# Kernel tuning notes

Measured on AMD Instinct MI355X. Metric: run time of the kernel, lower is better.

The kernel has to match this reference:

```python
import jax, jax.numpy as jnp
import numpy as np

TOL = 0.5          # Time_tolerance
DECAY = 1.0        # decay_rate
RES = 0.03         # integral_resolution
T_MAX = 120.0
G = 4000           # int(T_MAX / RES)


def setup_inputs() -> dict:
    key = jax.random.key(0)
    ks = jax.random.split(key, 8)
    B, N, H = 128, 64, 128
    times0 = jnp.sort(jax.random.uniform(ks[0], (B, N), dtype=jnp.float32) * T_MAX, axis=-1)
    times1 = jnp.sort(jax.random.uniform(ks[1], (B, N), dtype=jnp.float32) * T_MAX, axis=-1)
    states0 = jax.random.randint(ks[2], (B, N), 0, 2, dtype=jnp.int32)
    states1 = jax.random.randint(ks[3], (B, N), 0, 2, dtype=jnp.int32)
    head_times = jnp.sort(jax.random.uniform(ks[4], (B, H), dtype=jnp.float32) * T_MAX, axis=-1)
    head_states = jax.random.randint(ks[5], (B, H), 0, 2, dtype=jnp.int32)
    base = jnp.full((1,), -0.2, dtype=jnp.float32)  # torch.ones(1) * -0.2
    weights = jax.random.normal(ks[6], (2,), dtype=jnp.float32) * 0.1
    return dict(times0=times0, states0=states0, times1=times1, states1=states1,
                head_times=head_times, head_states=head_states, base=base, weights=weights)


def _intensity(t, times0, states0, times1, states1, head_times, head_states, base, wn):
    # t: [B,T] evaluation times; times*: [B,N]; head_*: [B,H]
    te = t[..., None]                                   # [B,T,1]
    t0 = times0[:, None, :]                             # [B,1,N]
    t1 = times1[:, None, :]
    s0 = states0[:, None, :]
    s1 = states1[:, None, :]
    # exp(-decay*(t - tau)); clamp dt>=0 so masked-out (future) events don't overflow
    dec0 = jnp.exp(-DECAY * jnp.maximum(te - t0, 0.0))  # [B,T,N]
    dec1 = jnp.exp(-DECAY * jnp.maximum(te - t1, 0.0))
    # Formula 0: body [0,1], signs [1,1], relations (0 BEFORE 1), (1 BEFORE head)
    A = jnp.where((t0 <= te) & (s0 == 1), dec0, 0.0)                 # history mask + kernel on pred0
    Bm = jnp.where((t1 < te - TOL) & (s1 == 1), dec1, 0.0)           # (t1 BEFORE head) + history mask
    M = (times0[:, :, None] - times1[:, None, :] < -TOL).astype(t.dtype)  # [B,N,N] (t0 BEFORE t1)
    feat0 = jnp.einsum('bti,bij,btj->bt', A, M, Bm)  # sum over itertools.product pairs
    # Formula 1: body [0], sign [0], relation (0 BEFORE head)
    feat1 = jnp.sum(jnp.where((t0 < te - TOL) & (s0 == 0), dec0, 0.0), axis=-1)
    # formula effect: cur_state via idx = sum(t > head_times) - 1 (numpy negative-index wrap)
    cnt = jnp.sum(te > head_times[:, None, :], axis=-1)              # [B,T]
    Hn = head_times.shape[-1]
    cur_state = jnp.take_along_axis(head_states, (cnt - 1) % Hn, axis=-1)
    eff0 = jnp.where(cur_state == 0, 1.0, -1.0).astype(t.dtype)      # head sign 1 -> +1 iff counter_state==1
    eff1 = -eff0                                                      # head sign 0
    return jnp.exp(base[0] + wn[0] * feat0 * eff0 + wn[1] * feat1 * eff1)


def reference(times0, states0, times1, states1, head_times, head_states, base, weights):
    wn = jax.nn.softmax(weights)  # exp(w)/sum exp(w)
    B = times0.shape[0]
    grid = jnp.broadcast_to((jnp.arange(G, dtype=times0.dtype) * RES)[None, :], (B, G))
    lam_grid = _intensity(grid, times0, states0, times1, states1, head_times, head_states, base, wn)
    lam_ev = _intensity(head_times[:, 1:], times0, states0, times1, states1, head_times, head_states, base, wn)
    log_sum = jnp.sum(jnp.log(lam_ev))
    integral = jnp.sum(lam_grid) * RES
    return (log_sum - integral).reshape(1)
```

## Files before the change

kernel.cpp:

```cpp
#include <hip/hip_runtime.h>
#include <math.h>

constexpr int Bb = 128;
constexpr int Nn = 64;
constexpr int Hh = 128;
constexpr int Gg = 4000;
constexpr float  TOLf = 0.5f;
constexpr double RESd = 0.03;

constexpr int GBLK  = 16;
constexpr int NGRID = Bb * GBLK;
constexpr int NBLK  = NGRID + Bb;
constexpr int TSTRIDE = 72;

__device__ __forceinline__ int lb64(const float* __restrict__ a, float key) {
    int lo = (a[31] < key) ? 32 : 0;
    lo += (a[lo + 15] < key) ? 16 : 0;
    lo += (a[lo + 7]  < key) ? 8  : 0;
    lo += (a[lo + 3]  < key) ? 4  : 0;
    lo += (a[lo + 1]  < key) ? 2  : 0;
    lo += (a[lo]      < key) ? 1  : 0;
    lo += (a[lo]      < key) ? 1  : 0;
    return lo;
}
__device__ __forceinline__ int ub64(const float* __restrict__ a, float key) {
    int lo = (a[31] <= key) ? 32 : 0;
    lo += (a[lo + 15] <= key) ? 16 : 0;
    lo += (a[lo + 7]  <= key) ? 8  : 0;
    lo += (a[lo + 3]  <= key) ? 4  : 0;
    lo += (a[lo + 1]  <= key) ? 2  : 0;
    lo += (a[lo]      <= key) ? 1  : 0;
    lo += (a[lo]      <= key) ? 1  : 0;
    return lo;
}
__device__ __forceinline__ int lb128(const float* __restrict__ a, float key) {
    int lo = (a[63] < key) ? 64 : 0;
    lo += (a[lo + 31] < key) ? 32 : 0;
    lo += (a[lo + 15] < key) ? 16 : 0;
    lo += (a[lo + 7]  < key) ? 8  : 0;
    lo += (a[lo + 3]  < key) ? 4  : 0;
    lo += (a[lo + 1]  < key) ? 2  : 0;
    lo += (a[lo]      < key) ? 1  : 0;
    lo += (a[lo]      < key) ? 1  : 0;
    return lo;
}

__global__ __launch_bounds__(64) void precompute_kernel(
    const float* __restrict__ times0, const int* __restrict__ states0,
    const float* __restrict__ times1, const int* __restrict__ states1,
    double* __restrict__ Ps_all, double* __restrict__ Qs_all,
    double* __restrict__ SW_all, double* __restrict__ SWP_all,
    int* __restrict__ kT_all)
{
    const int b = blockIdx.x;
    const int i = threadIdx.x;

    __shared__ float  t1s[Nn];
    __shared__ int    j0s[Nn];
    __shared__ double Ps_sh[Nn + 1];

    const float t0 = times0[b * Nn + i];
    const float t1 = times1[b * Nn + i];
    const int   s0 = states0[b * Nn + i];
    const int   s1 = states1[b * Nn + i];
    t1s[i] = t1;
    __syncthreads();

    int j0 = 0;
    #pragma unroll
    for (int j = 0; j < Nn; ++j)
        j0 += (t0 - t1s[j] >= -TOLf) ? 1 : 0;
    j0s[i] = j0;

    const double e0 = exp((double)t0);
    double vp = (s1 == 1) ? exp((double)t1) : 0.0;
    double vq = (s0 == 0) ? e0 : 0.0;
    const double W = (s0 == 1) ? e0 : 0.0;
    double vw = W;

    #pragma unroll
    for (int off = 1; off < 64; off <<= 1) {
        double op = __shfl_up(vp, off, 64);
        double oq = __shfl_up(vq, off, 64);
        double ow = __shfl_up(vw, off, 64);
        if (i >= off) { vp += op; vq += oq; vw += ow; }
    }
    Ps_sh[i + 1] = vp;
    if (i == 0) Ps_sh[0] = 0.0;
    __syncthreads();

    double vwp = W * Ps_sh[j0];
    #pragma unroll
    for (int off = 1; off < 64; off <<= 1) {
        double o = __shfl_up(vwp, off, 64);
        if (i >= off) vwp += o;
    }

    int kc = 0;
    #pragma unroll
    for (int j = 0; j < Nn; ++j)
        kc += (j0s[j] <= i) ? 1 : 0;

    double* Ps  = Ps_all  + b * TSTRIDE;
    double* Qs  = Qs_all  + b * TSTRIDE;
    double* SW  = SW_all  + b * TSTRIDE;
    double* SWP = SWP_all + b * TSTRIDE;
    int*    kT  = kT_all  + b * TSTRIDE;

    Ps[i + 1]  = vp;  Qs[i + 1]  = vq;
    SW[i + 1]  = vw;  SWP[i + 1] = vwp;
    kT[i] = kc;
    if (i == 0) {
        Ps[0] = 0.0; Qs[0] = 0.0; SW[0] = 0.0; SWP[0] = 0.0;
        kT[Nn] = Nn;
    }
}

__global__ __launch_bounds__(256) void eval_kernel(
    const float* __restrict__ times0, const float* __restrict__ times1,
    const float* __restrict__ head_times, const int* __restrict__ head_states,
    const float* __restrict__ base, const float* __restrict__ weights,
    const double* __restrict__ Ps_all, const double* __restrict__ Qs_all,
    const double* __restrict__ SW_all, const double* __restrict__ SWP_all,
    const int* __restrict__ kT_all,
    double* __restrict__ partials)
{
    __shared__ float  t0s[Nn], t1s[Nn];
    __shared__ float  hts[Hh];
    __shared__ int    hss[Hh];
    __shared__ double Ps[Nn + 1], Qs[Nn + 1], SW[Nn + 1], SWP[Nn + 1];
    __shared__ int    kT[Nn + 1];
    __shared__ double wsh[3];
    __shared__ double redsh[4];

    const int tid = threadIdx.x;
    const bool isEvent = blockIdx.x >= (unsigned)NGRID;
    const int b     = isEvent ? (blockIdx.x - NGRID) : (blockIdx.x >> 4);
    const int gbase = isEvent ? 0 : ((blockIdx.x & 15) << 8);
    const double tbase = (double)gbase * 0.03;

    if (tid < Nn) {
        t0s[tid] = times0[b * Nn + tid];
        t1s[tid] = times1[b * Nn + tid];
    } else if (tid < 192) {
        const int k = tid - 64;
        hts[k] = head_times[b * Hh + k];
        hss[k] = head_states[b * Hh + k];
    } else {
        const double sE = isEvent ? 1.0 : exp(-tbase);
        int k = tid - 192;
        const int base_i = b * TSTRIDE;
        Ps[k]  = Ps_all [base_i + k] * sE;
        Qs[k]  = Qs_all [base_i + k] * sE;
        SW[k]  = SW_all [base_i + k] * sE;
        SWP[k] = SWP_all[base_i + k] * (sE * sE);
        kT[k]  = kT_all [base_i + k];
        if (tid == 192) {
            k = Nn;
            Ps[k]  = Ps_all [base_i + k] * sE;
            Qs[k]  = Qs_all [base_i + k] * sE;
            SW[k]  = SW_all [base_i + k] * sE;
            SWP[k] = SWP_all[base_i + k] * (sE * sE);
            kT[k]  = kT_all [base_i + k];
        }
    }
    if (tid == 0) {
        const double w0 = (double)weights[0], w1 = (double)weights[1];
        const double mw = fmax(w0, w1);
        const double e0 = exp(w0 - mw), e1 = exp(w1 - mw);
        wsh[0] = e0 / (e0 + e1);
        wsh[1] = e1 / (e0 + e1);
        wsh[2] = (double)base[0];
    }
    __syncthreads();

    double contrib = 0.0;

    if (isEvent) {
        if (tid >= 1 && tid < Hh) {
            const float tf = hts[tid];
            const float thr = tf - TOLf;
            const int c   = lb64(t1s, thr);
            const int c0  = lb64(t0s, thr);
            const int c1  = ub64(t0s, tf);
            const int cnt = lb128(hts, tf);

            const int m = min(c1, kT[c]);
            const double a  = Ps[c] * SW[m] - SWP[m];
            const double ed = exp(-(double)tf);
            const double f0 = a * ed * ed;
            const double f1 = Qs[c0] * ed;
            const int cur = hss[((unsigned)(cnt - 1)) & (unsigned)(Hh - 1)];
            const double eff = (cur == 0) ? 1.0 : -1.0;
            contrib = wsh[2] + eff * (wsh[0] * f0 - wsh[1] * f1);
        }
    } else {
        const int g = gbase + tid;
        if (g < Gg) {
            const float tf = (float)g * 0.03f;
            const float thr = tf - TOLf;
            const int c   = lb64(t1s, thr);
            const int c0  = lb64(t0s, thr);
            const int c1  = ub64(t0s, tf);
            const int cnt = lb128(hts, tf);

            const int m = min(c1, kT[c]);
            const double a = Ps[c] * SW[m] - SWP[m];
            const double dt = (double)tf - tbase;
            const float f0 = (float)a * __expf((float)(-2.0 * dt));
            const float f1 = (float)Qs[c0] * __expf((float)(-dt));
            const int cur = hss[((unsigned)(cnt - 1)) & (unsigned)(Hh - 1)];
            const float eff = (cur == 0) ? 1.0f : -1.0f;
            const float ll = (float)wsh[2] + eff * ((float)wsh[0] * f0 - (float)wsh[1] * f1);
            contrib = -RESd * (double)__expf(ll);
        }
    }

    double v = contrib;
    #pragma unroll
    for (int off = 32; off > 0; off >>= 1) v += __shfl_down(v, off, 64);
    if ((tid & 63) == 0) redsh[tid >> 6] = v;
    __syncthreads();
    if (tid == 0) partials[blockIdx.x] = redsh[0] + redsh[1] + redsh[2] + redsh[3];
}

__global__ __launch_bounds__(256) void finalize_kernel(
    const double* __restrict__ partials, float* __restrict__ out)
{
    __shared__ double redsh[4];
    const int tid = threadIdx.x;
    double v = 0.0;
    for (int i = tid; i < NBLK; i += 256) v += partials[i];
    #pragma unroll
    for (int off = 32; off > 0; off >>= 1) v += __shfl_down(v, off, 64);
    if ((tid & 63) == 0) redsh[tid >> 6] = v;
    __syncthreads();
    if (tid == 0) out[0] = (float)(redsh[0] + redsh[1] + redsh[2] + redsh[3]);
}

extern "C" void kernel_launch(void* const* d_in, const int* in_sizes, int n_in,
                              void* d_out, int out_size, void* d_ws, size_t ws_size,
                              hipStream_t stream) {
    const float* times0      = (const float*)d_in[0];
    const int*   states0     = (const int*)  d_in[1];
    const float* times1      = (const float*)d_in[2];
    const int*   states1     = (const int*)  d_in[3];
    const float* head_times  = (const float*)d_in[4];
    const int*   head_states = (const int*)  d_in[5];
    const float* base        = (const float*)d_in[6];
    const float* weights     = (const float*)d_in[7];

    double* Ps_all  = (double*)d_ws;
    double* Qs_all  = Ps_all  + Bb * TSTRIDE;
    double* SW_all  = Qs_all  + Bb * TSTRIDE;
    double* SWP_all = SW_all  + Bb * TSTRIDE;
    int*    kT_all  = (int*)(SWP_all + Bb * TSTRIDE);
    double* partials = (double*)(kT_all + Bb * TSTRIDE);

    precompute_kernel<<<Bb, 64, 0, stream>>>(times0, states0, times1, states1,
                                             Ps_all, Qs_all, SW_all, SWP_all, kT_all);
    eval_kernel<<<NBLK, 256, 0, stream>>>(times0, times1, head_times, head_states,
                                          base, weights,
                                          Ps_all, Qs_all, SW_all, SWP_all, kT_all,
                                          partials);
    finalize_kernel<<<1, 256, 0, stream>>>(partials, (float*)d_out);
}
```

Baseline: 77.64 us.

## Fuse finalize into eval via last-block ticket and halve grid blocks

Removes the separate finalize kernel launch: each eval block writes its partial, bumps an atomic ticket, and the last block reduces all partials and writes the output. The softmax of weights moves into the precompute kernel, which also resets the ticket. Grid blocks per batch drop from 16 to 8, so each thread handles two grid points. This saves one launch and per-block setup, at the cost of an atomic and a serialized final reduction in the last block.

Result: slower. 97.71 us (+25.8%).

```diff
diff --git a/kernel.cpp b/kernel.cpp
--- a/kernel.cpp
+++ b/kernel.cpp
@@ -8,7 +8,7 @@
 constexpr float  TOLf = 0.5f;
 constexpr double RESd = 0.03;
 
-constexpr int GBLK  = 16;
+constexpr int GBLK  = 8;
 constexpr int NGRID = Bb * GBLK;
 constexpr int NBLK  = NGRID + Bb;
 constexpr int TSTRIDE = 72;
@@ -48,9 +48,11 @@
 __global__ __launch_bounds__(64) void precompute_kernel(
     const float* __restrict__ times0, const int* __restrict__ states0,
     const float* __restrict__ times1, const int* __restrict__ states1,
+    const float* __restrict__ base, const float* __restrict__ weights,
     double* __restrict__ Ps_all, double* __restrict__ Qs_all,
     double* __restrict__ SW_all, double* __restrict__ SWP_all,
-    int* __restrict__ kT_all)
+    int* __restrict__ kT_all,
+    double* __restrict__ hdr, int* __restrict__ ticket)
 {
     const int b = blockIdx.x;
     const int i = threadIdx.x;
@@ -114,29 +116,38 @@
         Ps[0] = 0.0; Qs[0] = 0.0; SW[0] = 0.0; SWP[0] = 0.0;
         kT[Nn] = Nn;
     }
+    if (b == 0 && i == 0) {
+        const double w0 = (double)weights[0], w1 = (double)weights[1];
+        const double mw = fmax(w0, w1);
+        const double ew0 = exp(w0 - mw), ew1 = exp(w1 - mw);
+        hdr[0] = ew0 / (ew0 + ew1);
+        hdr[1] = ew1 / (ew0 + ew1);
+        hdr[2] = (double)base[0];
+        *ticket = 0;
+    }
 }
 
 __global__ __launch_bounds__(256) void eval_kernel(
     const float* __restrict__ times0, const float* __restrict__ times1,
     const float* __restrict__ head_times, const int* __restrict__ head_states,
-    const float* __restrict__ base, const float* __restrict__ weights,
     const double* __restrict__ Ps_all, const double* __restrict__ Qs_all,
     const double* __restrict__ SW_all, const double* __restrict__ SWP_all,
     const int* __restrict__ kT_all,
-    double* __restrict__ partials)
+    const double* __restrict__ hdr, int* __restrict__ ticket,
+    double* __restrict__ partials, float* __restrict__ out)
 {
     __shared__ float  t0s[Nn], t1s[Nn];
     __shared__ float  hts[Hh];
     __shared__ int    hss[Hh];
     __shared__ double Ps[Nn + 1], Qs[Nn + 1], SW[Nn + 1], SWP[Nn + 1];
     __shared__ int    kT[Nn + 1];
-    __shared__ double wsh[3];
     __shared__ double redsh[4];
+    __shared__ int    amLast;
 
     const int tid = threadIdx.x;
     const bool isEvent = blockIdx.x >= (unsigned)NGRID;
-    const int b     = isEvent ? (blockIdx.x - NGRID) : (blockIdx.x >> 4);
-    const int gbase = isEvent ? 0 : ((blockIdx.x & 15) << 8);
+    const int b     = isEvent ? (blockIdx.x - NGRID) : (blockIdx.x >> 3);
+    const int gbase = isEvent ? 0 : ((blockIdx.x & 7) << 9);
     const double tbase = (double)gbase * 0.03;
 
     if (tid < Nn) {
@@ -164,15 +175,9 @@
             kT[k]  = kT_all [base_i + k];
         }
     }
-    if (tid == 0) {
-        const double w0 = (double)weights[0], w1 = (double)weights[1];
-        const double mw = fmax(w0, w1);
-        const double e0 = exp(w0 - mw), e1 = exp(w1 - mw);
-        wsh[0] = e0 / (e0 + e1);
-        wsh[1] = e1 / (e0 + e1);
-        wsh[2] = (double)base[0];
-    }
-    __syncthreads();
+    __syncthreads();
+
+    const double wn0 = hdr[0], wn1 = hdr[1], bse = hdr[2];
 
     double contrib = 0.0;
 
@@ -192,27 +197,31 @@
             const double f1 = Qs[c0] * ed;
             const int cur = hss[((unsigned)(cnt - 1)) & (unsigned)(Hh - 1)];
             const double eff = (cur == 0) ? 1.0 : -1.0;
-            contrib = wsh[2] + eff * (wsh[0] * f0 - wsh[1] * f1);
+            contrib = bse + eff * (wn0 * f0 - wn1 * f1);
         }
     } else {
-        const int g = gbase + tid;
-        if (g < Gg) {
-            const float tf = (float)g * 0.03f;
-            const float thr = tf - TOLf;
-            const int c   = lb64(t1s, thr);
-            const int c0  = lb64(t0s, thr);
-            const int c1  = ub64(t0s, tf);
-            const int cnt = lb128(hts, tf);
-
-            const int m = min(c1, kT[c]);
-            const double a = Ps[c] * SW[m] - SWP[m];
-            const double dt = (double)tf - tbase;
-            const float f0 = (float)a * __expf((float)(-2.0 * dt));
-            const float f1 = (float)Qs[c0] * __expf((float)(-dt));
-            const int cur = hss[((unsigned)(cnt - 1)) & (unsigned)(Hh - 1)];
-            const float eff = (cur == 0) ? 1.0f : -1.0f;
-            const float ll = (float)wsh[2] + eff * ((float)wsh[0] * f0 - (float)wsh[1] * f1);
-            contrib = -RESd * (double)__expf(ll);
+        const float fw0 = (float)wn0, fw1 = (float)wn1, fbse = (float)bse;
+        #pragma unroll
+        for (int pp = 0; pp < 2; ++pp) {
+            const int g = gbase + tid + pp * 256;
+            if (g < Gg) {
+                const float tf = (float)g * 0.03f;
+                const float thr = tf - TOLf;
+                const int c   = lb64(t1s, thr);
+                const int c0  = lb64(t0s, thr);
+                const int c1  = ub64(t0s, tf);
+                const int cnt = lb128(hts, tf);
+
+                const int m = min(c1, kT[c]);
+                const double a = Ps[c] * SW[m] - SWP[m];
+                const double dt = (double)tf - tbase;
+                const float f0 = (float)a * __expf((float)(-2.0 * dt));
+                const float f1 = (float)Qs[c0] * __expf((float)(-dt));
+                const int cur = hss[((unsigned)(cnt - 1)) & (unsigned)(Hh - 1)];
+                const float eff = (cur == 0) ? 1.0f : -1.0f;
+                const float ll = fbse + eff * (fw0 * f0 - fw1 * f1);
+                contrib += -RESd * (double)__expf(ll);
+            }
         }
     }
 
@@ -221,21 +230,24 @@
     for (int off = 32; off > 0; off >>= 1) v += __shfl_down(v, off, 64);
     if ((tid & 63) == 0) redsh[tid >> 6] = v;
     __syncthreads();
-    if (tid == 0) partials[blockIdx.x] = redsh[0] + redsh[1] + redsh[2] + redsh[3];
-}
-
-__global__ __launch_bounds__(256) void finalize_kernel(
-    const double* __restrict__ partials, float* __restrict__ out)
-{
-    __shared__ double redsh[4];
-    const int tid = threadIdx.x;
-    double v = 0.0;
-    for (int i = tid; i < NBLK; i += 256) v += partials[i];
-    #pragma unroll
-    for (int off = 32; off > 0; off >>= 1) v += __shfl_down(v, off, 64);
-    if ((tid & 63) == 0) redsh[tid >> 6] = v;
-    __syncthreads();
-    if (tid == 0) out[0] = (float)(redsh[0] + redsh[1] + redsh[2] + redsh[3]);
+    if (tid == 0) {
+        partials[blockIdx.x] = redsh[0] + redsh[1] + redsh[2] + redsh[3];
+        __threadfence();
+        const int old = atomicAdd(ticket, 1);
+        amLast = (old == NBLK - 1) ? 1 : 0;
+    }
+    __syncthreads();
+
+    if (amLast) {
+        __threadfence();
+        double s = 0.0;
+        for (int i = tid; i < NBLK; i += 256) s += partials[i];
+        #pragma unroll
+        for (int off = 32; off > 0; off >>= 1) s += __shfl_down(s, off, 64);
+        if ((tid & 63) == 0) redsh[tid >> 6] = s;
+        __syncthreads();
+        if (tid == 0) out[0] = (float)(redsh[0] + redsh[1] + redsh[2] + redsh[3]);
+    }
 }
 
 extern "C" void kernel_launch(void* const* d_in, const int* in_sizes, int n_in,
@@ -255,13 +267,15 @@
     double* SW_all  = Qs_all  + Bb * TSTRIDE;
     double* SWP_all = SW_all  + Bb * TSTRIDE;
     int*    kT_all  = (int*)(SWP_all + Bb * TSTRIDE);
-    double* partials = (double*)(kT_all + Bb * TSTRIDE);
+    double* hdr     = (double*)(kT_all + Bb * TSTRIDE);
+    int*    ticket  = (int*)(hdr + 4);
+    double* partials = hdr + 6;
 
     precompute_kernel<<<Bb, 64, 0, stream>>>(times0, states0, times1, states1,
-                                             Ps_all, Qs_all, SW_all, SWP_all, kT_all);
+                                             base, weights,
+                                             Ps_all, Qs_all, SW_all, SWP_all, kT_all,
+                                             hdr, ticket);
     eval_kernel<<<NBLK, 256, 0, stream>>>(times0, times1, head_times, head_states,
-                                          base, weights,
                                           Ps_all, Qs_all, SW_all, SWP_all, kT_all,
-                                          partials);
-    finalize_kernel<<<1, 256, 0, stream>>>(partials, (float*)d_out);
-}
+                                          hdr, ticket, partials, (float*)d_out);
+}
```

## Fuse per-batch prefix-sum precompute into eval kernel, dropping a launch

Applied to the files above, without the earlier changes.

Removes the separate precompute kernel and has each eval block recompute its batch's prefix sums (Ps, Qs, SW, SWP, kT) in shared memory with its first wavefront. The per-block exp(-tbase) scaling is folded into the exponentials at build time. This drops one kernel launch and its global-memory round trip. In exchange, the per-batch scan and the O(N^2) counting loops are now repeated 17 times per batch (once per block), and the binary searches are hoisted before the scan so they can overlap it.

Result: no change. 78.67 us (+1.3%).

```diff
diff --git a/kernel.cpp b/kernel.cpp
--- a/kernel.cpp
+++ b/kernel.cpp
@@ -11,7 +11,6 @@
 constexpr int GBLK  = 16;
 constexpr int NGRID = Bb * GBLK;
 constexpr int NBLK  = NGRID + Bb;
-constexpr int TSTRIDE = 72;
 
 __device__ __forceinline__ int lb64(const float* __restrict__ a, float key) {
     int lo = (a[31] < key) ? 32 : 0;
@@ -45,84 +44,11 @@
     return lo;
 }
 
-__global__ __launch_bounds__(64) void precompute_kernel(
+__global__ __launch_bounds__(256) void eval_kernel(
     const float* __restrict__ times0, const int* __restrict__ states0,
     const float* __restrict__ times1, const int* __restrict__ states1,
-    double* __restrict__ Ps_all, double* __restrict__ Qs_all,
-    double* __restrict__ SW_all, double* __restrict__ SWP_all,
-    int* __restrict__ kT_all)
-{
-    const int b = blockIdx.x;
-    const int i = threadIdx.x;
-
-    __shared__ float  t1s[Nn];
-    __shared__ int    j0s[Nn];
-    __shared__ double Ps_sh[Nn + 1];
-
-    const float t0 = times0[b * Nn + i];
-    const float t1 = times1[b * Nn + i];
-    const int   s0 = states0[b * Nn + i];
-    const int   s1 = states1[b * Nn + i];
-    t1s[i] = t1;
-    __syncthreads();
-
-    int j0 = 0;
-    #pragma unroll
-    for (int j = 0; j < Nn; ++j)
-        j0 += (t0 - t1s[j] >= -TOLf) ? 1 : 0;
-    j0s[i] = j0;
-
-    const double e0 = exp((double)t0);
-    double vp = (s1 == 1) ? exp((double)t1) : 0.0;
-    double vq = (s0 == 0) ? e0 : 0.0;
-    const double W = (s0 == 1) ? e0 : 0.0;
-    double vw = W;
-
-    #pragma unroll
-    for (int off = 1; off < 64; off <<= 1) {
-        double op = __shfl_up(vp, off, 64);
-        double oq = __shfl_up(vq, off, 64);
-        double ow = __shfl_up(vw, off, 64);
-        if (i >= off) { vp += op; vq += oq; vw += ow; }
-    }
-    Ps_sh[i + 1] = vp;
-    if (i == 0) Ps_sh[0] = 0.0;
-    __syncthreads();
-
-    double vwp = W * Ps_sh[j0];
-    #pragma unroll
-    for (int off = 1; off < 64; off <<= 1) {
-        double o = __shfl_up(vwp, off, 64);
-        if (i >= off) vwp += o;
-    }
-
-    int kc = 0;
-    #pragma unroll
-    for (int j = 0; j < Nn; ++j)
-        kc += (j0s[j] <= i) ? 1 : 0;
-
-    double* Ps  = Ps_all  + b * TSTRIDE;
-    double* Qs  = Qs_all  + b * TSTRIDE;
-    double* SW  = SW_all  + b * TSTRIDE;
-    double* SWP = SWP_all + b * TSTRIDE;
-    int*    kT  = kT_all  + b * TSTRIDE;
-
-    Ps[i + 1]  = vp;  Qs[i + 1]  = vq;
-    SW[i + 1]  = vw;  SWP[i + 1] = vwp;
-    kT[i] = kc;
-    if (i == 0) {
-        Ps[0] = 0.0; Qs[0] = 0.0; SW[0] = 0.0; SWP[0] = 0.0;
-        kT[Nn] = Nn;
-    }
-}
-
-__global__ __launch_bounds__(256) void eval_kernel(
-    const float* __restrict__ times0, const float* __restrict__ times1,
     const float* __restrict__ head_times, const int* __restrict__ head_states,
     const float* __restrict__ base, const float* __restrict__ weights,
-    const double* __restrict__ Ps_all, const double* __restrict__ Qs_all,
-    const double* __restrict__ SW_all, const double* __restrict__ SWP_all,
-    const int* __restrict__ kT_all,
     double* __restrict__ partials)
 {
     __shared__ float  t0s[Nn], t1s[Nn];
@@ -130,6 +56,7 @@
     __shared__ int    hss[Hh];
     __shared__ double Ps[Nn + 1], Qs[Nn + 1], SW[Nn + 1], SWP[Nn + 1];
     __shared__ int    kT[Nn + 1];
+    __shared__ int    j0s[Nn];
     __shared__ double wsh[3];
     __shared__ double redsh[4];
 
@@ -141,75 +68,101 @@
 
     if (tid < Nn) {
         t0s[tid] = times0[b * Nn + tid];
-        t1s[tid] = times1[b * Nn + tid];
-    } else if (tid < 192) {
-        const int k = tid - 64;
+    } else if (tid < 128) {
+        t1s[tid - 64] = times1[b * Nn + (tid - 64)];
+    } else {
+        const int k = tid - 128;
         hts[k] = head_times[b * Hh + k];
         hss[k] = head_states[b * Hh + k];
+    }
+    __syncthreads();
+
+    float tf = 0.0f;
+    bool active = false;
+    if (isEvent) {
+        if (tid >= 1 && tid < Hh) { tf = hts[tid]; active = true; }
     } else {
+        const int g = gbase + tid;
+        if (g < Gg) { tf = (float)g * 0.03f; active = true; }
+    }
+    int c = 0, c0 = 0, c1 = 0, cnt = 0;
+    if (active) {
+        const float thr = tf - TOLf;
+        c   = lb64(t1s, thr);
+        c0  = lb64(t0s, thr);
+        c1  = ub64(t0s, tf);
+        cnt = lb128(hts, tf);
+    }
+
+    if (tid < Nn) {
+        const int i = tid;
+        const float t0 = t0s[i];
+        const float t1 = t1s[i];
+        const int   s0 = states0[b * Nn + i];
+        const int   s1 = states1[b * Nn + i];
+
+        int j0 = 0;
+        #pragma unroll
+        for (int j = 0; j < Nn; ++j)
+            j0 += (t0 - t1s[j] >= -TOLf) ? 1 : 0;
+        j0s[i] = j0;
+
         const double sE = isEvent ? 1.0 : exp(-tbase);
-        int k = tid - 192;
-        const int base_i = b * TSTRIDE;
-        Ps[k]  = Ps_all [base_i + k] * sE;
-        Qs[k]  = Qs_all [base_i + k] * sE;
-        SW[k]  = SW_all [base_i + k] * sE;
-        SWP[k] = SWP_all[base_i + k] * (sE * sE);
-        kT[k]  = kT_all [base_i + k];
-        if (tid == 192) {
-            k = Nn;
-            Ps[k]  = Ps_all [base_i + k] * sE;
-            Qs[k]  = Qs_all [base_i + k] * sE;
-            SW[k]  = SW_all [base_i + k] * sE;
-            SWP[k] = SWP_all[base_i + k] * (sE * sE);
-            kT[k]  = kT_all [base_i + k];
+        const double e0 = exp((double)t0) * sE;
+        double vp = (s1 == 1) ? exp((double)t1) * sE : 0.0;
+        double vq = (s0 == 0) ? e0 : 0.0;
+        const double W = (s0 == 1) ? e0 : 0.0;
+        double vw = W;
+
+        #pragma unroll
+        for (int off = 1; off < 64; off <<= 1) {
+            double op = __shfl_up(vp, off, 64);
+            double oq = __shfl_up(vq, off, 64);
+            double ow = __shfl_up(vw, off, 64);
+            if (i >= off) { vp += op; vq += oq; vw += ow; }
         }
-    }
-    if (tid == 0) {
+        Ps[i + 1] = vp;  Qs[i + 1] = vq;  SW[i + 1] = vw;
+        if (i == 0) { Ps[0] = 0.0; Qs[0] = 0.0; SW[0] = 0.0; SWP[0] = 0.0; kT[Nn] = Nn; }
+
+        double vwp = W * Ps[j0];
+        #pragma unroll
+        for (int off = 1; off < 64; off <<= 1) {
+            double o = __shfl_up(vwp, off, 64);
+            if (i >= off) vwp += o;
+        }
+        SWP[i + 1] = vwp;
+
+        int kc = 0;
+        #pragma unroll
+        for (int j = 0; j < Nn; ++j)
+            kc += (j0s[j] <= i) ? 1 : 0;
+        kT[i] = kc;
+    } else if (tid == 64) {
         const double w0 = (double)weights[0], w1 = (double)weights[1];
         const double mw = fmax(w0, w1);
-        const double e0 = exp(w0 - mw), e1 = exp(w1 - mw);
-        wsh[0] = e0 / (e0 + e1);
-        wsh[1] = e1 / (e0 + e1);
+        const double ew0 = exp(w0 - mw), ew1 = exp(w1 - mw);
+        wsh[0] = ew0 / (ew0 + ew1);
+        wsh[1] = ew1 / (ew0 + ew1);
         wsh[2] = (double)base[0];
     }
     __syncthreads();
 
     double contrib = 0.0;
-
-    if (isEvent) {
-        if (tid >= 1 && tid < Hh) {
-            const float tf = hts[tid];
-            const float thr = tf - TOLf;
-            const int c   = lb64(t1s, thr);
-            const int c0  = lb64(t0s, thr);
-            const int c1  = ub64(t0s, tf);
-            const int cnt = lb128(hts, tf);
-
-            const int m = min(c1, kT[c]);
+    if (active) {
+        const int m = min(c1, kT[c]);
+        const int cur = hss[((unsigned)(cnt - 1)) & (unsigned)(Hh - 1)];
+        if (isEvent) {
             const double a  = Ps[c] * SW[m] - SWP[m];
             const double ed = exp(-(double)tf);
             const double f0 = a * ed * ed;
             const double f1 = Qs[c0] * ed;
-            const int cur = hss[((unsigned)(cnt - 1)) & (unsigned)(Hh - 1)];
             const double eff = (cur == 0) ? 1.0 : -1.0;
             contrib = wsh[2] + eff * (wsh[0] * f0 - wsh[1] * f1);
-        }
-    } else {
-        const int g = gbase + tid;
-        if (g < Gg) {
-            const float tf = (float)g * 0.03f;
-            const float thr = tf - TOLf;
-            const int c   = lb64(t1s, thr);
-            const int c0  = lb64(t0s, thr);
-            const int c1  = ub64(t0s, tf);
-            const int cnt = lb128(hts, tf);
-
-            const int m = min(c1, kT[c]);
+        } else {
             const double a = Ps[c] * SW[m] - SWP[m];
             const double dt = (double)tf - tbase;
             const float f0 = (float)a * __expf((float)(-2.0 * dt));
             const float f1 = (float)Qs[c0] * __expf((float)(-dt));
-            const int cur = hss[((unsigned)(cnt - 1)) & (unsigned)(Hh - 1)];
             const float eff = (cur == 0) ? 1.0f : -1.0f;
             const float ll = (float)wsh[2] + eff * ((float)wsh[0] * f0 - (float)wsh[1] * f1);
             contrib = -RESd * (double)__expf(ll);
@@ -250,18 +203,10 @@
     const float* base        = (const float*)d_in[6];
     const float* weights     = (const float*)d_in[7];
 
-    double* Ps_all  = (double*)d_ws;
-    double* Qs_all  = Ps_all  + Bb * TSTRIDE;
-    double* SW_all  = Qs_all  + Bb * TSTRIDE;
-    double* SWP_all = SW_all  + Bb * TSTRIDE;
-    int*    kT_all  = (int*)(SWP_all + Bb * TSTRIDE);
-    double* partials = (double*)(kT_all + Bb * TSTRIDE);
-
-    precompute_kernel<<<Bb, 64, 0, stream>>>(times0, states0, times1, states1,
-                                             Ps_all, Qs_all, SW_all, SWP_all, kT_all);
-    eval_kernel<<<NBLK, 256, 0, stream>>>(times0, times1, head_times, head_states,
-                                          base, weights,
-                                          Ps_all, Qs_all, SW_all, SWP_all, kT_all,
+    double* partials = (double*)d_ws;
+
+    eval_kernel<<<NBLK, 256, 0, stream>>>(times0, states0, times1, states1,
+                                          head_times, head_states, base, weights,
                                           partials);
     finalize_kernel<<<1, 256, 0, stream>>>(partials, (float*)d_out);
 }
```
